# Kernel optimization log

Hardware: AMD Instinct MI355X
Metric: run time of the kernel (lower is better)

## Reference

```python
import jax, jax.numpy as jnp
import numpy as np

EPS = 1e-5

def setup_inputs() -> dict:
    key = jax.random.key(0)
    ks = jax.random.split(key, 12)
    B, L, d_model, d_pair = 2, 384, 1024, 128
    h = jax.random.normal(ks[0], (B, L, d_model), dtype=jnp.float32)
    # torch.nn.Linear params: W [out,in], b [out]
    Wi = jax.random.normal(ks[1], (d_pair, d_model), dtype=jnp.float32) * 0.02
    bi = jnp.zeros((d_pair,), dtype=jnp.float32)
    Wj = jax.random.normal(ks[2], (d_pair, d_model), dtype=jnp.float32) * 0.02
    bj = jnp.zeros((d_pair,), dtype=jnp.float32)
    bilinear_weight = jax.random.normal(ks[3], (d_pair, d_pair, d_pair), dtype=jnp.float32) * 0.02
    gamma = jnp.ones((d_pair,), dtype=jnp.float32)
    beta = jnp.zeros((d_pair,), dtype=jnp.float32)
    mix_w = jax.random.normal(ks[4], (d_pair, d_pair, 3, 3), dtype=jnp.float32) * 0.02  # OIHW
    out_w = jax.random.normal(ks[5], (d_pair, d_pair, 1, 1), dtype=jnp.float32) * 0.05
    out_b = jnp.zeros((d_pair,), dtype=jnp.float32)
    return {"h": h, "Wi": Wi, "bi": bi, "Wj": Wj, "bj": bj,
            "bilinear_weight": bilinear_weight, "gamma": gamma, "beta": beta,
            "mix_w": mix_w, "out_w": out_w, "out_b": out_b}

def _instance_norm(x, gamma, beta):
    # x: [B, C, H, W]; normalize per (b, c) over spatial dims
    mean = jnp.mean(x, axis=(2, 3), keepdims=True)
    var = jnp.var(x, axis=(2, 3), keepdims=True)
    xn = (x - mean) * jax.lax.rsqrt(var + EPS)
    return xn * gamma[None, :, None, None] + beta[None, :, None, None]

def _conv(x, w):
    return jax.lax.conv_general_dilated(
        x, w, window_strides=(1, 1), padding='SAME',
        dimension_numbers=('NCHW', 'OIHW', 'NCHW'))

def reference(h, Wi, bi, Wj, bj, bilinear_weight, gamma, beta, mix_w, out_w, out_b):
    ui = h @ Wi.T + bi  # [B, L, d_pair]
    vj = h @ Wj.T + bj  # [B, L, d_pair]
    # pairwise bilinear: [B, d_pair(k), L, L]
    feat = jnp.einsum('bli,ijk,bmj->bklm', ui, bilinear_weight, vj)
    feat = _instance_norm(feat, gamma, beta)
    feat = jax.nn.relu(feat)
    feat = jax.nn.relu(_conv(feat, mix_w))
    return _conv(feat, out_w) + out_b[None, :, None, None]
```

## Files before the change

kernel.cpp:

```cpp
#include <hip/hip_runtime.h>
#include <hip/hip_bf16.h>
#include <stdint.h>

typedef __bf16 bf16_t;
typedef __bf16 bf16x8 __attribute__((ext_vector_type(8)));
typedef float  f32x4  __attribute__((ext_vector_type(4)));

#define MFMA(a, b, c) __builtin_amdgcn_mfma_f32_16x16x32_bf16((a), (b), (c), 0, 0, 0)

__device__ __forceinline__ void gload_lds16(const void* g, void* l) {
  __builtin_amdgcn_global_load_lds(
      (const __attribute__((address_space(1))) unsigned int*)(g),
      (__attribute__((address_space(3))) unsigned int*)(l), 16, 0, 0);
}

__global__ __launch_bounds__(256) void k_lin2(
    const float* __restrict__ h, const float* __restrict__ Wi,
    const float* __restrict__ bi, const float* __restrict__ Wj,
    const float* __restrict__ bj, bf16_t* __restrict__ ui,
    bf16_t* __restrict__ vj) {
  int m0 = blockIdx.x * 64;
  int which = blockIdx.y;
  const float* W = which ? Wj : Wi;
  const float* bias = which ? bj : bi;
  bf16_t* out = which ? vj : ui;
  __shared__ bf16_t Al[64][136];
  __shared__ bf16_t Bl[128][136];
  int w = threadIdx.x >> 6, ln = threadIdx.x & 63;
  int wr = (w >> 1) * 32, wc = (w & 1) * 64;
  int lr = ln & 15, hi8 = (ln >> 4) * 8, rb = (ln >> 4) * 4;
  f32x4 acc[2][4] = {};
  for (int kc0 = 0; kc0 < 1024; kc0 += 128) {
    __syncthreads();
    for (int c = threadIdx.x; c < 64 * 16; c += 256) {
      int row = c >> 4, col = (c & 15) * 8;
      const float* src = &h[(size_t)(m0 + row) * 1024 + kc0 + col];
      f32x4 a = *(const f32x4*)src, b2 = *(const f32x4*)(src + 4);
      bf16x8 o;
#pragma unroll
      for (int e = 0; e < 4; e++) {
        o[e] = (bf16_t)a[e];
        o[e + 4] = (bf16_t)b2[e];
      }
      *(bf16x8*)&Al[row][col] = o;
    }
    for (int c = threadIdx.x; c < 128 * 16; c += 256) {
      int row = c >> 4, col = (c & 15) * 8;
      const float* src = &W[(size_t)row * 1024 + kc0 + col];
      f32x4 a = *(const f32x4*)src, b2 = *(const f32x4*)(src + 4);
      bf16x8 o;
#pragma unroll
      for (int e = 0; e < 4; e++) {
        o[e] = (bf16_t)a[e];
        o[e + 4] = (bf16_t)b2[e];
      }
      *(bf16x8*)&Bl[row][col] = o;
    }
    __syncthreads();
#pragma unroll
    for (int kc = 0; kc < 128; kc += 32) {
      bf16x8 a0 = *(bf16x8*)&Al[wr + lr][kc + hi8];
      bf16x8 a1 = *(bf16x8*)&Al[wr + 16 + lr][kc + hi8];
#pragma unroll
      for (int fn = 0; fn < 4; fn++) {
        bf16x8 bv = *(bf16x8*)&Bl[wc + fn * 16 + lr][kc + hi8];
        acc[0][fn] = MFMA(a0, bv, acc[0][fn]);
        acc[1][fn] = MFMA(a1, bv, acc[1][fn]);
      }
    }
  }
#pragma unroll
  for (int fm = 0; fm < 2; fm++)
#pragma unroll
    for (int fn = 0; fn < 4; fn++) {
      int col = wc + fn * 16 + lr;
      float bb = bias[col];
#pragma unroll
      for (int r = 0; r < 4; r++) {
        int row = m0 + wr + fm * 16 + rb + r;
        out[row * 128 + col] = (bf16_t)(acc[fm][fn][r] + bb);
      }
    }
}

__global__ __launch_bounds__(256) void k_wt(const float* __restrict__ W,
                                            bf16_t* __restrict__ Wt) {
  int j = blockIdx.x;
  int i0 = blockIdx.y * 32, k0 = blockIdx.z * 32;
  __shared__ float tile[32][33];
  int tx = threadIdx.x & 31, ty = threadIdx.x >> 5;
#pragma unroll
  for (int r = 0; r < 4; r++) {
    int ii = ty + r * 8;
    tile[ii][tx] = W[(size_t)(i0 + ii) * 16384 + j * 128 + (k0 + tx)];
  }
  __syncthreads();
#pragma unroll
  for (int r = 0; r < 4; r++) {
    int kk = ty + r * 8;
    Wt[(size_t)(k0 + kk) * 16384 + j * 128 + (i0 + tx)] = (bf16_t)tile[tx][kk];
  }
}

__global__ __launch_bounds__(256) void k_wc(const float* __restrict__ mw,
                                            bf16_t* __restrict__ Wc2) {
  int idx = blockIdx.x * 256 + threadIdx.x;
  if (idx < 147456) {
    int e = idx & 7, ln = (idx >> 3) & 63, fm = (idx >> 9) & 3;
    int kc = (idx >> 11) & 3, wrh = (idx >> 13) & 1, tap = idx >> 14;
    int oc = wrh * 64 + fm * 16 + (ln & 15);
    int ic = kc * 32 + (ln >> 4) * 8 + e;
    Wc2[idx] = (bf16_t)mw[oc * 1152 + ic * 9 + tap];
  }
}

__global__ __launch_bounds__(256) void k_wo(const float* __restrict__ ow,
                                            bf16_t* __restrict__ Wo2) {
  int idx = blockIdx.x * 256 + threadIdx.x;
  if (idx < 16384) {
    int e = idx & 7, ln = (idx >> 3) & 63, fm = (idx >> 9) & 3;
    int kc = (idx >> 11) & 3, wrh = (idx >> 13) & 1;
    int oc2 = wrh * 64 + fm * 16 + (ln & 15);
    int mc = kc * 32 + (ln >> 4) * 8 + e;
    Wo2[idx] = (bf16_t)ow[oc2 * 128 + mc];
  }
}

__global__ __launch_bounds__(256) void k_tgemm(const bf16_t* __restrict__ A,
                                               const bf16_t* __restrict__ Bt,
                                               bf16_t* __restrict__ T) {
  int m0 = blockIdx.x * 64;
  int n0 = blockIdx.y * 64;
  __shared__ bf16_t Al[64][136], Bl[64][136];
  for (int c = threadIdx.x; c < 64 * 16; c += 256) {
    int row = c >> 4, col = (c & 15) * 8;
    *(uint4*)&Al[row][col] = *(const uint4*)&A[(size_t)(m0 + row) * 128 + col];
    *(uint4*)&Bl[row][col] = *(const uint4*)&Bt[(size_t)(n0 + row) * 128 + col];
  }
  __syncthreads();
  int w = threadIdx.x >> 6, ln = threadIdx.x & 63;
  int wr = (w >> 1) * 32, wc = (w & 1) * 32;
  int lr = ln & 15, hi8 = (ln >> 4) * 8, rb = (ln >> 4) * 4;
  f32x4 acc[2][2] = {};
#pragma unroll
  for (int kc = 0; kc < 128; kc += 32) {
    bf16x8 a0 = *(bf16x8*)&Al[wr + lr][kc + hi8];
    bf16x8 a1 = *(bf16x8*)&Al[wr + 16 + lr][kc + hi8];
    bf16x8 b0 = *(bf16x8*)&Bl[wc + lr][kc + hi8];
    bf16x8 b1 = *(bf16x8*)&Bl[wc + 16 + lr][kc + hi8];
    acc[0][0] = MFMA(a0, b0, acc[0][0]);
    acc[0][1] = MFMA(a0, b1, acc[0][1]);
    acc[1][0] = MFMA(a1, b0, acc[1][0]);
    acc[1][1] = MFMA(a1, b1, acc[1][1]);
  }
#pragma unroll
  for (int fm = 0; fm < 2; fm++)
#pragma unroll
    for (int fn = 0; fn < 2; fn++) {
      int col = n0 + wc + fn * 16 + lr;
#pragma unroll
      for (int r = 0; r < 4; r++) {
        int row = m0 + wr + fm * 16 + rb + r;
        T[(size_t)row * 16384 + col] = (bf16_t)acc[fm][fn][r];
      }
    }
}

__global__ __launch_bounds__(256) void k_feat(const bf16_t* __restrict__ T,
                                              const bf16_t* __restrict__ Vb,
                                              bf16_t* __restrict__ F,
                                              float* __restrict__ part) {
  int bl = blockIdx.x;
  int b = bl / 384;
  __shared__ __align__(16) char sm[52224];
  bf16_t (*Tl)[136] = (bf16_t(*)[136])(sm);
  bf16_t (*Fb)[136] = (bf16_t(*)[136])(sm + 34816);
  float* rs = (float*)(sm);
  float* rq = (float*)(sm + 8192);
  const bf16_t* tsrc = T + (size_t)bl * 16384;
  for (int c = threadIdx.x; c < 128 * 16; c += 256) {
    int row = c >> 4, col = (c & 15) * 8;
    *(uint4*)&Tl[row][col] = *(const uint4*)&tsrc[row * 128 + col];
  }
  __syncthreads();
  int w = threadIdx.x >> 6, ln = threadIdx.x & 63;
  int wr = (w >> 1) * 64, wc = (w & 1) * 32;
  int lr = ln & 15, g = ln >> 4, hi8 = g * 8, rb = g * 4;
  size_t base = (size_t)bl * 384 * 128;
  float s8[8] = {}, q8[8] = {};
  int col8 = threadIdx.x & 15;
  for (int mt = 0; mt < 6; mt++) {
    bf16x8 vf[2][4];
#pragma unroll
    for (int fn = 0; fn < 2; fn++)
#pragma unroll
      for (int kc = 0; kc < 4; kc++) {
        int m = mt * 64 + wc + fn * 16 + lr;
        vf[fn][kc] = *(const bf16x8*)&Vb[(size_t)(b * 384 + m) * 128 +
                                         kc * 32 + hi8];
      }
    f32x4 acc[4][2] = {};
#pragma unroll
    for (int kc = 0; kc < 4; kc++) {
#pragma unroll
      for (int fm = 0; fm < 4; fm++) {
        bf16x8 av = *(bf16x8*)&Tl[wr + fm * 16 + lr][kc * 32 + hi8];
        acc[fm][0] = MFMA(av, vf[0][kc], acc[fm][0]);
        acc[fm][1] = MFMA(av, vf[1][kc], acc[fm][1]);
      }
    }
    __syncthreads();
    union {
      bf16_t h[4];
      uint2 u;
    } pk;
#pragma unroll
    for (int fm = 0; fm < 4; fm++)
#pragma unroll
      for (int fn = 0; fn < 2; fn++) {
        int m = wc + fn * 16 + lr;
        int kb = wr + fm * 16 + rb;
#pragma unroll
        for (int r = 0; r < 4; r++) pk.h[r] = (bf16_t)acc[fm][fn][r];
        *(uint2*)&Fb[m][kb] = pk.u;
      }
    __syncthreads();
    for (int c = threadIdx.x; c < 64 * 16; c += 256) {
      int row = c >> 4;
      uint4 v = *(uint4*)&Fb[row][col8 * 8];
      *(uint4*)&F[base + (size_t)(mt * 64 + row) * 128 + col8 * 8] = v;
      const bf16_t* hp = (const bf16_t*)&v;
#pragma unroll
      for (int e = 0; e < 8; e++) {
        float f = (float)hp[e];
        s8[e] += f;
        q8[e] += f * f;
      }
    }
  }
  int sub = threadIdx.x >> 4;
#pragma unroll
  for (int e = 0; e < 8; e++) {
    rs[(sub * 16 + col8) * 8 + e] = s8[e];
    rq[(sub * 16 + col8) * 8 + e] = q8[e];
  }
  __syncthreads();
  if (threadIdx.x < 128) {
    int k = threadIdx.x, kg = k >> 3, e = k & 7;
    float S = 0.f, Q = 0.f;
#pragma unroll
    for (int s = 0; s < 16; s++) {
      S += rs[(s * 16 + kg) * 8 + e];
      Q += rq[(s * 16 + kg) * 8 + e];
    }
    part[(size_t)bl * 256 + k] = S;
    part[(size_t)bl * 256 + 128 + k] = Q;
  }
}

__global__ __launch_bounds__(64) void k_stats2(const float* __restrict__ part,
                                               const float* __restrict__ gamma,
                                               const float* __restrict__ beta,
                                               float* __restrict__ ss) {
  int k = blockIdx.x, b = blockIdx.y, t = threadIdx.x;
  float S = 0.f, Q = 0.f;
  for (int l = t; l < 384; l += 64) {
    S += part[(size_t)(b * 384 + l) * 256 + k];
    Q += part[(size_t)(b * 384 + l) * 256 + 128 + k];
  }
#pragma unroll
  for (int o = 32; o; o >>= 1) {
    S += __shfl_down(S, o, 64);
    Q += __shfl_down(Q, o, 64);
  }
  if (t == 0) {
    const float inv = 1.0f / 147456.0f;
    float mean = S * inv;
    float var = Q * inv - mean * mean;
    float sc = gamma[k] * rsqrtf(var + 1e-5f);
    ss[b * 256 + k] = sc;
    ss[b * 256 + 128 + k] = beta[k] - mean * sc;
  }
}

__global__ __launch_bounds__(256, 2) void k_conv(
    const bf16_t* __restrict__ Fn, const float* __restrict__ ss,
    const bf16_t* __restrict__ Wc2, const bf16_t* __restrict__ Wo2,
    const float* __restrict__ outb, float* __restrict__ out) {
  int orig = blockIdx.x;
  int wg = (orig & 7) * 288 + (orig >> 3);
  int xt = wg % 3;
  int t1 = wg / 3;
  int b = t1 / 384;
  int y = t1 - b * 384;
  int x0 = xt * 128;

  __shared__ __align__(16) char sm[66048];
  char* smB = sm + 32768;

  int tid = threadIdx.x;
  int w = tid >> 6, ln = tid & 63;
  int wrh = w >> 1, pxb = (w & 1) * 64;
  int lr = ln & 15, g = ln >> 4, rb = g * 4;

  int c8 = (tid & 15) * 8;
  float scr[8], shr[8];
  {
    const float* sb = ss + b * 256;
    *(f32x4*)&scr[0] = *(const f32x4*)&sb[c8];
    *(f32x4*)&scr[4] = *(const f32x4*)&sb[c8 + 4];
    *(f32x4*)&shr[0] = *(const f32x4*)&sb[128 + c8];
    *(f32x4*)&shr[4] = *(const f32x4*)&sb[128 + c8 + 4];
  }

  f32x4 acc[4][4] = {};
  for (int dy = 0; dy < 3; dy++) {
    int yy = y + dy - 1;
    bool yok = (yy >= 0 && yy < 384);
    __syncthreads();
    const char* Frow = (const char*)Fn + (size_t)(b * 384 + yy) * 98304;
#pragma unroll
    for (int i = 0; i < 9; i++) {
      int s = tid + i * 256;
      if (s < 2080) {
        int px = s >> 4, c16 = (s & 15) << 4;
        int xx = x0 - 1 + px;
        bf16x8 o;
        if (yok && xx >= 0 && xx < 384) {
          bf16x8 f = *(const bf16x8*)(Frow + (size_t)xx * 256 + c16);
#pragma unroll
          for (int e = 0; e < 8; e++) {
            float v = (float)f[e] * scr[e] + shr[e];
            o[e] = (bf16_t)(v > 0.f ? v : 0.f);
          }
        } else {
#pragma unroll
          for (int e = 0; e < 8; e++) o[e] = (bf16_t)0.f;
        }
        int byte = (px << 8) + c16;
        *(bf16x8*)(smB + (byte ^ ((px & 7) << 4))) = o;
      }
    }
#pragma unroll
    for (int dx = 0; dx < 3; dx++) {
      if (dx) __syncthreads();
      const char* WcTap = (const char*)Wc2 + (size_t)(dy * 3 + dx) * 32768;
#pragma unroll
      for (int i = 0; i < 8; i++) {
        int o4 = w * 8192 + i * 1024 + ln * 16;
        gload_lds16(WcTap + o4, sm + o4);
      }
      __syncthreads();
#pragma unroll
      for (int kc = 0; kc < 4; kc++) {
        bf16x8 av[4], bv[4];
#pragma unroll
        for (int fn = 0; fn < 4; fn++) {
          int row = pxb + fn * 16 + lr + dx;
          int byte = (row << 8) + (kc << 6) + (g << 4);
          bv[fn] = *(const bf16x8*)(smB + (byte ^ ((row & 7) << 4)));
        }
#pragma unroll
        for (int fm = 0; fm < 4; fm++)
          av[fm] = *(const bf16x8*)(sm + wrh * 16384 + kc * 4096 + fm * 1024 +
                                    ln * 16);
#pragma unroll
        for (int fm = 0; fm < 4; fm++)
#pragma unroll
          for (int fn = 0; fn < 4; fn++)
            acc[fm][fn] = MFMA(av[fm], bv[fn], acc[fm][fn]);
      }
    }
  }
  __syncthreads();
#pragma unroll
  for (int i = 0; i < 8; i++) {
    int o4 = w * 8192 + i * 1024 + ln * 16;
    gload_lds16((const char*)Wo2 + o4, sm + o4);
  }
  union {
    bf16_t hh[4];
    uint2 u;
  } pk;
#pragma unroll
  for (int fm = 0; fm < 4; fm++)
#pragma unroll
    for (int fn = 0; fn < 4; fn++) {
      int px = pxb + fn * 16 + lr;
      int mcb = wrh * 64 + fm * 16 + rb;
#pragma unroll
      for (int r = 0; r < 4; r++) {
        float v = acc[fm][fn][r];
        pk.hh[r] = (bf16_t)(v > 0.f ? v : 0.f);
      }
      int byte = (px << 8) + (mcb << 1);
      *(uint2*)(smB + (byte ^ ((px & 7) << 4))) = pk.u;
    }
  __syncthreads();
  f32x4 acc2[4][4] = {};
#pragma unroll
  for (int kc = 0; kc < 4; kc++) {
    bf16x8 av[4], bv[4];
#pragma unroll
    for (int fn = 0; fn < 4; fn++) {
      int row = pxb + fn * 16 + lr;
      int byte = (row << 8) + (kc << 6) + (g << 4);
      bv[fn] = *(const bf16x8*)(smB + (byte ^ ((row & 7) << 4)));
    }
#pragma unroll
    for (int fm = 0; fm < 4; fm++)
      av[fm] = *(const bf16x8*)(sm + wrh * 16384 + kc * 4096 + fm * 1024 +
                                ln * 16);
#pragma unroll
    for (int fm = 0; fm < 4; fm++)
#pragma unroll
      for (int fn = 0; fn < 4; fn++)
        acc2[fm][fn] = MFMA(av[fm], bv[fn], acc2[fm][fn]);
  }
  f32x4 obv[4];
#pragma unroll
  for (int fm = 0; fm < 4; fm++)
    obv[fm] = *(const f32x4*)&outb[wrh * 64 + fm * 16 + rb];
#pragma unroll
  for (int fm = 0; fm < 4; fm++)
#pragma unroll
    for (int fn = 0; fn < 4; fn++) {
      int x = x0 + pxb + fn * 16 + lr;
#pragma unroll
      for (int r = 0; r < 4; r++) {
        int oc2 = wrh * 64 + fm * 16 + rb + r;
        out[((size_t)(b * 128 + oc2) * 384 + y) * 384 + x] =
            acc2[fm][fn][r] + obv[fm][r];
      }
    }
}

extern "C" void kernel_launch(void* const* d_in, const int* in_sizes, int n_in,
                              void* d_out, int out_size, void* d_ws,
                              size_t ws_size, hipStream_t stream) {
  const float* h = (const float*)d_in[0];
  const float* Wi = (const float*)d_in[1];
  const float* bi = (const float*)d_in[2];
  const float* Wj = (const float*)d_in[3];
  const float* bj = (const float*)d_in[4];
  const float* Wbl = (const float*)d_in[5];
  const float* gamma = (const float*)d_in[6];
  const float* beta = (const float*)d_in[7];
  const float* mw = (const float*)d_in[8];
  const float* ow = (const float*)d_in[9];
  const float* ob = (const float*)d_in[10];
  float* out = (float*)d_out;

  char* ws = (char*)d_ws;
  size_t off = 0;
  auto alloc = [&](size_t bytes) -> void* {
    void* p = ws + off;
    off = (off + bytes + 255) & ~(size_t)255;
    return p;
  };
  bf16_t* ui_b = (bf16_t*)alloc(768 * 128 * 2);
  bf16_t* vj_b = (bf16_t*)alloc(768 * 128 * 2);
  bf16_t* Wt = (bf16_t*)alloc((size_t)2097152 * 2);
  bf16_t* Wc2 = (bf16_t*)alloc((size_t)147456 * 2);
  bf16_t* Wo2 = (bf16_t*)alloc((size_t)16384 * 2);
  bf16_t* T = (bf16_t*)alloc((size_t)768 * 16384 * 2);
  bf16_t* F = (bf16_t*)alloc((size_t)2 * 384 * 384 * 128 * 2);
  float* part = (float*)alloc((size_t)768 * 256 * 4);
  float* ssb = (float*)alloc((size_t)2 * 256 * 4);

  k_lin2<<<dim3(12, 2), 256, 0, stream>>>(h, Wi, bi, Wj, bj, ui_b, vj_b);
  k_wt<<<dim3(128, 4, 4), 256, 0, stream>>>(Wbl, Wt);
  k_wc<<<(147456 + 255) / 256, 256, 0, stream>>>(mw, Wc2);
  k_wo<<<64, 256, 0, stream>>>(ow, Wo2);
  k_tgemm<<<dim3(12, 256), 256, 0, stream>>>(ui_b, Wt, T);
  k_feat<<<768, 256, 0, stream>>>(T, vj_b, F, part);
  k_stats2<<<dim3(128, 2), 64, 0, stream>>>(part, gamma, beta, ssb);
  k_conv<<<2304, 256, 0, stream>>>(F, ssb, Wc2, Wo2, ob, out);
}
```

Baseline: 210.2 us.

## Double-buffer conv weight taps in LDS with async prefetch and explicit waits

Result: slower. 273.2 us (+30.0%).

```diff
diff --git a/kernel.cpp b/kernel.cpp
--- a/kernel.cpp
+++ b/kernel.cpp
@@ -7,6 +7,19 @@
 typedef float  f32x4  __attribute__((ext_vector_type(4)));
 
 #define MFMA(a, b, c) __builtin_amdgcn_mfma_f32_16x16x32_bf16((a), (b), (c), 0, 0, 0)
+
+#define WAITV(N)                                           \
+  {                                                        \
+    asm volatile("s_waitcnt vmcnt(" #N ")" ::: "memory");  \
+    __builtin_amdgcn_sched_barrier(0);                     \
+  }
+
+__device__ __forceinline__ void bar_sync() {
+  asm volatile("s_waitcnt lgkmcnt(0)" ::: "memory");
+  __builtin_amdgcn_sched_barrier(0);
+  __builtin_amdgcn_s_barrier();
+  __builtin_amdgcn_sched_barrier(0);
+}
 
 __device__ __forceinline__ void gload_lds16(const void* g, void* l) {
   __builtin_amdgcn_global_load_lds(
@@ -283,7 +296,7 @@
   }
 }
 
-__global__ __launch_bounds__(256, 2) void k_conv(
+__global__ __launch_bounds__(256, 1) void k_conv(
     const bf16_t* __restrict__ Fn, const float* __restrict__ ss,
     const bf16_t* __restrict__ Wc2, const bf16_t* __restrict__ Wo2,
     const float* __restrict__ outb, float* __restrict__ out) {
@@ -295,8 +308,8 @@
   int y = t1 - b * 384;
   int x0 = xt * 128;
 
-  __shared__ __align__(16) char sm[66048];
-  char* smB = sm + 32768;
+  __shared__ __align__(16) char sm[98816];
+  char* smB = sm + 65536;
 
   int tid = threadIdx.x;
   int w = tid >> 6, ln = tid & 63;
@@ -313,11 +326,24 @@
     *(f32x4*)&shr[4] = *(const f32x4*)&sb[128 + c8 + 4];
   }
 
+  auto issueA = [&](int t) {
+    const char* src = (t < 9) ? (const char*)Wc2 + (size_t)t * 32768
+                              : (const char*)Wo2;
+    char* dst = sm + (t & 1) * 32768;
+#pragma unroll
+    for (int i = 0; i < 8; i++) {
+      int o4 = w * 8192 + i * 1024 + ln * 16;
+      gload_lds16(src + o4, dst + o4);
+    }
+  };
+
+  issueA(0);
+  issueA(1);
+
   f32x4 acc[4][4] = {};
   for (int dy = 0; dy < 3; dy++) {
     int yy = y + dy - 1;
     bool yok = (yy >= 0 && yy < 384);
-    __syncthreads();
     const char* Frow = (const char*)Fn + (size_t)(b * 384 + yy) * 98304;
 #pragma unroll
     for (int i = 0; i < 9; i++) {
@@ -343,14 +369,10 @@
     }
 #pragma unroll
     for (int dx = 0; dx < 3; dx++) {
-      if (dx) __syncthreads();
-      const char* WcTap = (const char*)Wc2 + (size_t)(dy * 3 + dx) * 32768;
-#pragma unroll
-      for (int i = 0; i < 8; i++) {
-        int o4 = w * 8192 + i * 1024 + ln * 16;
-        gload_lds16(WcTap + o4, sm + o4);
-      }
-      __syncthreads();
+      int t = dy * 3 + dx;
+      WAITV(8);
+      bar_sync();
+      char* Ab = sm + (t & 1) * 32768;
 #pragma unroll
       for (int kc = 0; kc < 4; kc++) {
         bf16x8 av[4], bv[4];
@@ -362,7 +384,7 @@
         }
 #pragma unroll
         for (int fm = 0; fm < 4; fm++)
-          av[fm] = *(const bf16x8*)(sm + wrh * 16384 + kc * 4096 + fm * 1024 +
+          av[fm] = *(const bf16x8*)(Ab + wrh * 16384 + kc * 4096 + fm * 1024 +
                                     ln * 16);
 #pragma unroll
         for (int fm = 0; fm < 4; fm++)
@@ -370,13 +392,9 @@
           for (int fn = 0; fn < 4; fn++)
             acc[fm][fn] = MFMA(av[fm], bv[fn], acc[fm][fn]);
       }
-    }
-  }
-  __syncthreads();
-#pragma unroll
-  for (int i = 0; i < 8; i++) {
-    int o4 = w * 8192 + i * 1024 + ln * 16;
-    gload_lds16((const char*)Wo2 + o4, sm + o4);
+      bar_sync();
+      if (t + 2 <= 9) issueA(t + 2);
+    }
   }
   union {
     bf16_t hh[4];
@@ -396,26 +414,30 @@
       int byte = (px << 8) + (mcb << 1);
       *(uint2*)(smB + (byte ^ ((px & 7) << 4))) = pk.u;
     }
-  __syncthreads();
+  WAITV(0);
+  bar_sync();
   f32x4 acc2[4][4] = {};
-#pragma unroll
-  for (int kc = 0; kc < 4; kc++) {
-    bf16x8 av[4], bv[4];
-#pragma unroll
-    for (int fn = 0; fn < 4; fn++) {
-      int row = pxb + fn * 16 + lr;
-      int byte = (row << 8) + (kc << 6) + (g << 4);
-      bv[fn] = *(const bf16x8*)(smB + (byte ^ ((row & 7) << 4)));
-    }
-#pragma unroll
-    for (int fm = 0; fm < 4; fm++)
-      av[fm] = *(const bf16x8*)(sm + wrh * 16384 + kc * 4096 + fm * 1024 +
-                                ln * 16);
-#pragma unroll
-    for (int fm = 0; fm < 4; fm++)
-#pragma unroll
-      for (int fn = 0; fn < 4; fn++)
-        acc2[fm][fn] = MFMA(av[fm], bv[fn], acc2[fm][fn]);
+  {
+    char* Ab = sm + 32768;
+#pragma unroll
+    for (int kc = 0; kc < 4; kc++) {
+      bf16x8 av[4], bv[4];
+#pragma unroll
+      for (int fn = 0; fn < 4; fn++) {
+        int row = pxb + fn * 16 + lr;
+        int byte = (row << 8) + (kc << 6) + (g << 4);
+        bv[fn] = *(const bf16x8*)(smB + (byte ^ ((row & 7) << 4)));
+      }
+#pragma unroll
+      for (int fm = 0; fm < 4; fm++)
+        av[fm] = *(const bf16x8*)(Ab + wrh * 16384 + kc * 4096 + fm * 1024 +
+                                  ln * 16);
+#pragma unroll
+      for (int fm = 0; fm < 4; fm++)
+#pragma unroll
+        for (int fn = 0; fn < 4; fn++)
+          acc2[fm][fn] = MFMA(av[fm], bv[fn], acc2[fm][fn]);
+    }
   }
   f32x4 obv[4];
 #pragma unroll
```
